# Kernel optimization log

Measured on AMD Instinct MI355X. Metric: run time of the kernel, lower is better.

## Reference

```python
import jax, jax.numpy as jnp
import numpy as np
import math

INF = 1e12  # constant.INFINITY_NUMBER in the original repo


def setup_inputs() -> dict:
    key = jax.random.key(0)
    ks = jax.random.split(key, 12)
    B, S, W, D = 16, 512, 8, 768
    M, Wm = 2, 64
    U, Wu = 32, 16
    V = 32000
    words = jax.random.randint(ks[0], (B, S, W), 0, V)
    masks = jax.random.randint(ks[1], (B, S, W), 0, 2).astype(bool)
    main = jax.random.randint(ks[2], (B, M, Wm), 0, V)
    main_mask = jax.random.randint(ks[3], (B, M, Wm), 0, 2).astype(bool)
    user = jax.random.randint(ks[4], (B, U, Wu), 0, V)
    user_mask = jax.random.randint(ks[5], (B, U, Wu), 0, 2).astype(bool)
    # sparse-ish dependency adjacency
    adj = (jax.random.uniform(ks[6], (B, S, S)) < 0.05).astype(jnp.float32)
    emb_weight = jax.random.normal(ks[7], (V, D), jnp.float32) * 0.02
    K_w = jax.random.normal(ks[8], (D, D), jnp.float32) * (1.0 / math.sqrt(D))
    K_b = jnp.zeros((D,), jnp.float32)
    Q_w = jax.random.normal(ks[9], (D, D), jnp.float32) * (1.0 / math.sqrt(D))
    Q_b = jnp.zeros((D,), jnp.float32)
    return {"words": words, "masks": masks, "main": main, "main_mask": main_mask,
            "user": user, "user_mask": user_mask, "adj": adj,
            "emb_weight": emb_weight, "K_w": K_w, "K_b": K_b, "Q_w": Q_w, "Q_b": Q_b}


def _masked_max(embs, mask, axis):
    # masked_fill(mask, -INF) -> max(axis) ; caller fixes residual -INF rows
    return jnp.max(jnp.where(mask[..., None], -INF, embs), axis=axis)


def reference(words, masks, main, main_mask, user, user_mask, adj,
              emb_weight, K_w, K_b, Q_w, Q_b):
    D = emb_weight.shape[1]

    word_embs = emb_weight[words]   # [B,S,W,D]
    main_embs = emb_weight[main]    # [B,M,Wm,D]
    user_embs = emb_weight[user]    # [B,U,Wu,D]

    # node mask from adjacency: True where node has no in/out edges
    mask = ((adj.sum(axis=2) + adj.sum(axis=1)) == 0)[:, :, None]  # [B,S,1]

    # main: masked max-pool over word pieces, zero fully-masked rows
    main_e = _masked_max(main_embs, main_mask, axis=2)             # [B,M,D]
    main_e = jnp.where(main_e == -INF, 0.0, main_e)

    # user: masked max-pool over word pieces then over users
    user_e = _masked_max(user_embs, user_mask, axis=2)             # [B,U,D]
    user_e = jnp.max(user_e, axis=1)                               # [B,D]
    user_e = jnp.where(user_e == -INF, 0.0, user_e)

    # token embeddings: masked max-pool over word pieces (no -INF fix in original)
    g = _masked_max(word_embs, masks, axis=2)                      # [B,S,D]

    # single-head attention: softmax(K g (Q g)^T / sqrt(D)) @ g
    key_ = g @ K_w.T + K_b                                         # [B,S,D]
    query = g @ Q_w.T + Q_b                                        # [B,S,D]
    scores = jnp.einsum('bsd,btd->bst', key_, query) / math.sqrt(D)
    dense_graph = jax.nn.softmax(scores, axis=2)                   # [B,S,S]
    gcn_out = jnp.einsum('bst,btd->bsd', dense_graph, g)           # [B,S,D]

    adj_sm = jax.nn.softmax(adj, axis=2)

    return (gcn_out, mask, dense_graph, adj_sm,
            jnp.squeeze(main_e), jnp.squeeze(user_e))
```

## Files before the change

kernel.cpp:

```cpp
#include <hip/hip_runtime.h>
#include <hip/hip_bf16.h>
#include <math.h>

static constexpr int Bn = 16, Sn = 512, Wn = 8, Dn = 768;
static constexpr int Mn_ = 2, WMn = 64;
static constexpr int Un = 32, WUn = 16;

#define INF_VAL 1e12f
#define INV_SQRT_D 0.03608439182435161f

static constexpr size_t OFF_GCN   = 0;
static constexpr size_t OFF_MASK  = 6291456;
static constexpr size_t OFF_DENSE = 6299648;
static constexpr size_t OFF_ADJ   = 10493952;
static constexpr size_t OFF_MAIN  = 14688256;
static constexpr size_t OFF_USER  = 14712832;

static constexpr size_t WSB_GBF     = 0;
static constexpr size_t WSB_GT      = 12582912;
static constexpr size_t WSB_DENSEBF = 25165824;
static constexpr size_t WSB_HBF     = 33554432;
static constexpr size_t WSB_KWT     = 46137344;
static constexpr size_t WSB_QWT     = 47316992;
static constexpr size_t WSB_MT      = 48496640;
static constexpr size_t WSB_PARTU   = 49676288;
static constexpr size_t WSB_PARTM   = 51249152;
static constexpr size_t WSB_KBAR    = 51642368;
static constexpr size_t WSB_QBAR    = 51648512;
static constexpr size_t WSB_U       = 51654656;
static constexpr size_t WSB_V       = 51660800;
static constexpr size_t WSB_VA      = 51666944;
static constexpr size_t WSB_VB      = 51673088;
static constexpr size_t WSB_CONSTS  = 51679232;
static constexpr size_t WSB_QS      = 51679296;
static constexpr size_t WSB_KQ      = 51712064;
static constexpr size_t WSB_GA      = 51744832;
static constexpr size_t WSB_GB      = 51777600;
static constexpr size_t WSB_COLSUM  = 51810368;
static constexpr size_t WSB_FLAGS   = 51843136;
static constexpr size_t WSB_ROWSUM  = 51875904;
static constexpr size_t WSB_UVU     = 51908672;
static constexpr size_t WSB_UVV     = 51957824;
static constexpr size_t WSB_UVA     = 52006976;
static constexpr size_t WSB_UVB     = 52056128;
static constexpr size_t WSB_RAWBF   = 52105280;

typedef __attribute__((ext_vector_type(8))) short short8;
typedef __attribute__((ext_vector_type(4))) float f32x4;

static __device__ __forceinline__ ushort f2bf(float f) {
    union { float f; unsigned u; } v; v.f = f;
    unsigned u = v.u;
    unsigned r = (u + 0x7FFFu + ((u >> 16) & 1u)) >> 16;
    return (ushort)r;
}

static __device__ __forceinline__ float bf2f(unsigned hi16) {
    union { unsigned u; float f; } v; v.u = hi16 << 16; return v.f;
}

static __device__ __forceinline__ void gload16(const void* g, void* lds) {
    __builtin_amdgcn_global_load_lds(
        (const __attribute__((address_space(1))) void*)g,
        (__attribute__((address_space(3))) void*)lds, 16, 0, 0);
}

static __device__ __forceinline__ void fmax4(float4& a, const float4& x) {
    a.x = fmaxf(a.x, x.x); a.y = fmaxf(a.y, x.y);
    a.z = fmaxf(a.z, x.z); a.w = fmaxf(a.w, x.w);
}

__global__ __launch_bounds__(256)
void fold1(const float* __restrict__ K_w, const float* __restrict__ K_b,
           const float* __restrict__ Q_w, const float* __restrict__ Q_b,
           double* __restrict__ kbar, double* __restrict__ qbar,
           ushort* __restrict__ KwbT, ushort* __restrict__ QwbT,
           float* __restrict__ colsum) {
    int blk = blockIdx.x, t = threadIdx.x;
    if (blk < 192) {
        int wv = t >> 6, lane = t & 63;
        int r = blk * 4 + wv;
        double sk = 0.0, sq = 0.0;
        for (int d = lane; d < Dn; d += 64) {
            sk += (double)K_w[(size_t)r * Dn + d];
            sq += (double)Q_w[(size_t)r * Dn + d];
        }
        #pragma unroll
        for (int off = 32; off > 0; off >>= 1) {
            sk += __shfl_down(sk, off, 64);
            sq += __shfl_down(sq, off, 64);
        }
        if (lane == 0) {
            kbar[r] = -1e12 * sk + (double)K_b[r];
            qbar[r] = -1e12 * sq + (double)Q_b[r];
        }
    } else if (blk < 1344) {
        int tt = blk - 192;
        const float* src = (tt < 576) ? K_w : Q_w;
        ushort* dst = (tt < 576) ? KwbT : QwbT;
        int t6 = (tt < 576) ? tt : tt - 576;
        int e0 = (t6 % 24) * 32, i0 = (t6 / 24) * 32;
        __shared__ ushort tile[32][33];
        int tx = t & 31, ty = t >> 5;
        #pragma unroll
        for (int i2 = 0; i2 < 4; ++i2)
            tile[ty + i2 * 8][tx] = f2bf(src[(size_t)(e0 + ty + i2 * 8) * Dn + i0 + tx]);
        __syncthreads();
        #pragma unroll
        for (int i2 = 0; i2 < 4; ++i2)
            dst[(size_t)(i0 + ty + i2 * 8) * Dn + e0 + tx] = tile[tx][ty + i2 * 8];
    } else {
        for (int i = t; i < Bn * Sn; i += 256) colsum[i] = 0.f;
    }
}

template<int OUT_BF16>
static __device__ __forceinline__
void gemm_device(const ushort* __restrict__ A, const ushort* __restrict__ B,
                 void* __restrict__ Cout, int bx, int by, int bz,
                 int Km, int lda, int ldb, int ldc,
                 long long sA, long long sB, long long sC,
                 ushort* As, ushort* Bs) {
    const ushort* Ab = A + (size_t)bz * sA;
    const ushort* Bb = B + (size_t)bz * sB;
    int i0 = by * 64, j0 = bx * 64;
    int tid = threadIdx.x;
    int lane = tid & 63, wv = tid >> 6;
    int wr = wv >> 1, wc = wv & 1;
    int ln15 = lane & 15, lkg = lane >> 4;
    int r4 = lane >> 4;
    int c16 = lane & 15;

    f32x4 acc[2][2] = {};

    for (int k0 = 0; k0 < Km; k0 += 128) {
        #pragma unroll
        for (int it = 0; it < 4; ++it) {
            int r = it * 16 + wv * 4 + r4;
            int cc = c16 ^ (r & 15);
            ushort* dstA = As + (it * 4096 + wv * 1024) / 2;
            gload16(Ab + (size_t)(i0 + r) * lda + k0 + cc * 8, dstA);
        }
        #pragma unroll
        for (int it = 0; it < 4; ++it) {
            int r = it * 16 + wv * 4 + r4;
            int cc = c16 ^ (r & 15);
            ushort* dstB = Bs + (it * 4096 + wv * 1024) / 2;
            gload16(Bb + (size_t)(j0 + r) * ldb + k0 + cc * 8, dstB);
        }
        __syncthreads();
        #pragma unroll
        for (int kh = 0; kh < 4; ++kh) {
            short8 af[2], bfr[2];
            int kc = kh * 4 + lkg;
            #pragma unroll
            for (int f = 0; f < 2; ++f) {
                int ra = wr * 32 + f * 16 + ln15;
                af[f] = *(const short8*)((const char*)As + ra * 256 + ((kc ^ (ra & 15)) << 4));
                int rb = wc * 32 + f * 16 + ln15;
                bfr[f] = *(const short8*)((const char*)Bs + rb * 256 + ((kc ^ (rb & 15)) << 4));
            }
            #pragma unroll
            for (int fa = 0; fa < 2; ++fa)
                #pragma unroll
                for (int fb = 0; fb < 2; ++fb)
                    acc[fa][fb] = __builtin_amdgcn_mfma_f32_16x16x32_bf16(
                        af[fa], bfr[fb], acc[fa][fb], 0, 0, 0);
        }
        __syncthreads();
    }

    #pragma unroll
    for (int fa = 0; fa < 2; ++fa) {
        #pragma unroll
        for (int fb = 0; fb < 2; ++fb) {
            int n = j0 + wc * 32 + fb * 16 + ln15;
            #pragma unroll
            for (int rr = 0; rr < 4; ++rr) {
                int m = i0 + wr * 32 + fa * 16 + lkg * 4 + rr;
                float val = acc[fa][fb][rr];
                if (OUT_BF16) {
                    ((ushort*)Cout)[(size_t)bz * sC + (size_t)m * ldc + n] = f2bf(val);
                } else {
                    ((float*)Cout)[(size_t)bz * sC + (size_t)m * ldc + n] = val;
                }
            }
        }
    }
}

template<int OUT_BF16>
__global__ __launch_bounds__(256)
void gemm_mfma(const ushort* __restrict__ A, const ushort* __restrict__ B,
               void* __restrict__ Cout,
               int Km, int lda, int ldb, int ldc,
               long long sA, long long sB, long long sC) {
    __shared__ ushort As[64 * 128];
    __shared__ ushort Bs[64 * 128];
    gemm_device<OUT_BF16>(A, B, Cout, blockIdx.x, blockIdx.y, blockIdx.z,
                          Km, lda, ldb, ldc, sA, sB, sC, As, Bs);
}

__global__ __launch_bounds__(256)
void adjuvmt_kernel(const float* __restrict__ adj, float* __restrict__ adjsm,
                    float* __restrict__ colsum, float* __restrict__ rowsum,
                    const float* __restrict__ K_w, const float* __restrict__ Q_w,
                    const float* __restrict__ K_b, const float* __restrict__ Q_b,
                    const double* __restrict__ kbar, const double* __restrict__ qbar,
                    double* __restrict__ uvu, double* __restrict__ uvv,
                    double* __restrict__ uva, double* __restrict__ uvb,
                    const ushort* __restrict__ QwbT, const ushort* __restrict__ KwbT,
                    ushort* __restrict__ Mt) {
    __shared__ ushort SB[16384];
    __shared__ float n1s[16];
    int blk = blockIdx.x;
    int t = threadIdx.x;
    if (blk < 24) {
        int id = blk * 256 + t;
        int c = id / 768;
        int j = id - c * 768;
        int e0 = c * 96;
        double su = 0.0, sv = 0.0, sa = 0.0, sb = 0.0;
        for (int e = e0; e < e0 + 96; ++e) {
            double kw = (double)K_w[(size_t)e * Dn + j];
            double qw = (double)Q_w[(size_t)e * Dn + j];
            su += kw * qbar[e];
            sv += qw * kbar[e];
            sa += kw * (double)Q_b[e];
            sb += qw * (double)K_b[e];
        }
        uvu[(size_t)c * Dn + j] = su;
        uvv[(size_t)c * Dn + j] = sv;
        uva[(size_t)c * Dn + j] = sa;
        uvb[(size_t)c * Dn + j] = sb;
        return;
    }
    if (blk < 168) {
        int g = blk - 24;
        gemm_device<1>(QwbT, KwbT, Mt, g % 12, g / 12, 0,
                       Dn, Dn, Dn, Dn, 0, 0, 0, SB, SB + 8192);
        return;
    }
    int ab = blk - 168;
    int b = ab >> 5, rc = ab & 31;
    const float* base = adj + ((size_t)b * Sn + rc * 16) * Sn;
    float* obase = adjsm + ((size_t)b * Sn + rc * 16) * Sn;
    const float EM1 = 0.36787944117144233f;
    const float EP1 = 2.718281828459045f;
    float (*rows)[512] = (float(*)[512])SB;
    #pragma unroll
    for (int r = 0; r < 16; ++r) {
        rows[r][t]       = base[(size_t)r * Sn + t];
        rows[r][t + 256] = base[(size_t)r * Sn + t + 256];
    }
    __syncthreads();
    int wv = t >> 6, lane = t & 63;
    #pragma unroll
    for (int rr2 = 0; rr2 < 4; ++rr2) {
        int r = wv * 4 + rr2;
        float s = 0.f;
        #pragma unroll
        for (int c = 0; c < 8; ++c) s += rows[r][lane + c * 64];
        #pragma unroll
        for (int off = 32; off > 0; off >>= 1) s += __shfl_down(s, off, 64);
        if (lane == 0) {
            n1s[r] = s;
            rowsum[(size_t)b * Sn + rc * 16 + r] = s;
        }
    }
    __syncthreads();
    float colacc0 = 0.f, colacc1 = 0.f;
    #pragma unroll
    for (int r = 0; r < 16; ++r) {
        float a0 = rows[r][t], a1 = rows[r][t + 256];
        colacc0 += a0; colacc1 += a1;
        float n1 = n1s[r];
        float e1, e0;
        if (n1 > 0.f) { e1 = 1.f; e0 = EM1; } else { e1 = EP1; e0 = 1.f; }
        float inv = 1.f / (n1 * e1 + (512.f - n1) * e0);
        obase[(size_t)r * Sn + t]       = (a0 == 1.f ? e1 : e0) * inv;
        obase[(size_t)r * Sn + t + 256] = (a1 == 1.f ? e1 : e0) * inv;
    }
    atomicAdd(&colsum[(size_t)b * Sn + t], colacc0);
    atomicAdd(&colsum[(size_t)b * Sn + t + 256], colacc1);
}

__global__ __launch_bounds__(64)
void uvred_consts(const double* __restrict__ uvu, const double* __restrict__ uvv,
                  const double* __restrict__ uva, const double* __restrict__ uvb,
                  const double* __restrict__ kbar, const double* __restrict__ qbar,
                  const float* __restrict__ K_b, const float* __restrict__ Q_b,
                  double* __restrict__ u, double* __restrict__ v,
                  double* __restrict__ va, double* __restrict__ vb,
                  double* __restrict__ consts) {
    int blk = blockIdx.x;
    int l = threadIdx.x;
    if (blk < 12) {
        int j = blk * 64 + l;
        double su = 0.0, sv = 0.0, sa = 0.0, sb = 0.0;
        #pragma unroll
        for (int c = 0; c < 8; ++c) {
            su += uvu[(size_t)c * Dn + j];
            sv += uvv[(size_t)c * Dn + j];
            sa += uva[(size_t)c * Dn + j];
            sb += uvb[(size_t)c * Dn + j];
        }
        u[j] = su; v[j] = sv; va[j] = sa; vb[j] = sb;
    } else {
        double c0 = 0.0, c1 = 0.0, c2 = 0.0, c3 = 0.0;
        for (int e = l; e < Dn; e += 64) {
            c0 += kbar[e] * (double)Q_b[e];
            c1 += kbar[e] * qbar[e];
            c2 += qbar[e] * (double)K_b[e];
            c3 += (double)K_b[e] * (double)Q_b[e];
        }
        #pragma unroll
        for (int off = 32; off > 0; off >>= 1) {
            c0 += __shfl_down(c0, off, 64);
            c1 += __shfl_down(c1, off, 64);
            c2 += __shfl_down(c2, off, 64);
            c3 += __shfl_down(c3, off, 64);
        }
        if (l == 0) { consts[0] = c0; consts[1] = c1; consts[2] = c2; consts[3] = c3; }
    }
}

__global__ __launch_bounds__(192)
void pool_g_s1(const int* __restrict__ words, const int* __restrict__ masks,
               const int* __restrict__ main_idx, const int* __restrict__ mmask,
               const int* __restrict__ user_idx, const int* __restrict__ umask,
               const float* __restrict__ emb,
               const double* __restrict__ u, const double* __restrict__ v,
               const double* __restrict__ va, const double* __restrict__ vb,
               const double* __restrict__ consts,
               ushort* __restrict__ gbf, float* __restrict__ qs,
               float* __restrict__ kq, float* __restrict__ ga,
               float* __restrict__ gb, int* __restrict__ flags,
               float* __restrict__ partM, float* __restrict__ partU) {
    int blk = blockIdx.x;
    int t = threadIdx.x;
    if (blk >= Bn * Sn) {
        int s1 = blk - Bn * Sn;
        const int *irow, *mrow;
        float* dst;
        if (s1 < 128) {
            int bm = s1 >> 2, ch = s1 & 3;
            irow = main_idx + (size_t)bm * WMn + ch * 16;
            mrow = mmask + (size_t)bm * WMn + ch * 16;
            dst = partM + (size_t)s1 * Dn;
        } else {
            int bu = s1 - 128;
            irow = user_idx + (size_t)bu * WUn;
            mrow = umask + (size_t)bu * WUn;
            dst = partU + (size_t)bu * Dn;
        }
        float4 acc = make_float4(-INF_VAL, -INF_VAL, -INF_VAL, -INF_VAL);
        #pragma unroll
        for (int w = 0; w < 16; ++w) {
            if (mrow[w] != 0) continue;
            float4 x = ((const float4*)(emb + (size_t)irow[w] * Dn))[t];
            fmax4(acc, x);
        }
        ((float4*)dst)[t] = acc;
        return;
    }
    int bs = blk;
    const int* wrow = words + (size_t)bs * Wn;
    const int* mrow = masks + (size_t)bs * Wn;
    float4 acc = make_float4(-INF_VAL, -INF_VAL, -INF_VAL, -INF_VAL);
    int nm = 0;
    #pragma unroll
    for (int w = 0; w < Wn; ++w) {
        int mk = mrow[w];
        nm += (mk != 0);
        if (mk != 0) continue;
        float4 x = ((const float4*)(emb + (size_t)wrow[w] * Dn))[t];
        fmax4(acc, x);
    }
    ushort4 o;
    o.x = f2bf(acc.x); o.y = f2bf(acc.y); o.z = f2bf(acc.z); o.w = f2bf(acc.w);
    ((ushort4*)(gbf + (size_t)bs * Dn))[t] = o;
    int j = t * 4;
    double dv = v[j] * (double)acc.x + v[j+1] * (double)acc.y
              + v[j+2] * (double)acc.z + v[j+3] * (double)acc.w;
    double du = u[j] * (double)acc.x + u[j+1] * (double)acc.y
              + u[j+2] * (double)acc.z + u[j+3] * (double)acc.w;
    double da = va[j] * (double)acc.x + va[j+1] * (double)acc.y
              + va[j+2] * (double)acc.z + va[j+3] * (double)acc.w;
    double db = vb[j] * (double)acc.x + vb[j+1] * (double)acc.y
              + vb[j+2] * (double)acc.z + vb[j+3] * (double)acc.w;
    #pragma unroll
    for (int off = 32; off > 0; off >>= 1) {
        dv += __shfl_down(dv, off, 64);
        du += __shfl_down(du, off, 64);
        da += __shfl_down(da, off, 64);
        db += __shfl_down(db, off, 64);
    }
    __shared__ double rr[12];
    if ((t & 63) == 0) {
        rr[t >> 6] = dv; rr[3 + (t >> 6)] = du;
        rr[6 + (t >> 6)] = da; rr[9 + (t >> 6)] = db;
    }
    __syncthreads();
    if (t == 0) {
        qs[bs] = (float)(rr[0] + rr[1] + rr[2] + consts[0]);
        kq[bs] = (float)(rr[3] + rr[4] + rr[5] + consts[2]);
        ga[bs] = (float)(rr[6] + rr[7] + rr[8]);
        gb[bs] = (float)(rr[9] + rr[10] + rr[11]);
        flags[bs] = (nm == Wn) ? 1 : 0;
    }
}

__global__ __launch_bounds__(256)
void midh_kernel(const ushort* __restrict__ gbf, const ushort* __restrict__ Mt,
                 ushort* __restrict__ hbf, ushort* __restrict__ gT,
                 const float* __restrict__ partM, const float* __restrict__ partU,
                 float* __restrict__ outM, float* __restrict__ outU,
                 const float* __restrict__ rowsum, const float* __restrict__ colsum,
                 float* __restrict__ maskout) {
    __shared__ ushort SB[16384];
    int blk = blockIdx.x;
    int t = threadIdx.x;
    if (blk < 1536) {
        gemm_device<1>(gbf, Mt, hbf, blk % 12, blk / 12, 0,
                       Dn, Dn, Dn, Dn, 0, 0, 0, SB, SB + 8192);
        return;
    }
    if (blk < 7680) {
        int bb = blk - 1536;
        ushort (*tile)[33] = (ushort(*)[33])SB;
        int b = bb / 384;
        int rem = bb - b * 384;
        int d0 = (rem % 24) * 32, s0 = (rem / 24) * 32;
        int tx = t & 31, ty = t >> 5;
        #pragma unroll
        for (int i = 0; i < 4; ++i)
            tile[ty + i * 8][tx] = gbf[((size_t)(b * Sn + s0 + ty + i * 8)) * Dn + d0 + tx];
        __syncthreads();
        #pragma unroll
        for (int i = 0; i < 4; ++i)
            gT[((size_t)(b * Dn + d0 + ty + i * 8)) * Sn + s0 + tx] = tile[tx][ty + i * 8];
        return;
    }
    if (blk >= 7728) {
        int i = (blk - 7728) * 256 + t;
        if (i < Bn * Sn)
            maskout[i] = ((rowsum[i] + colsum[i]) == 0.f) ? 1.f : 0.f;
        return;
    }
    if (t >= 192) return;
    float4 acc = make_float4(-INF_VAL, -INF_VAL, -INF_VAL, -INF_VAL);
    float* dst;
    if (blk < 7712) {
        int bm = blk - 7680;
        #pragma unroll
        for (int c = 0; c < 4; ++c) {
            float4 x = ((const float4*)(partM + (size_t)(bm * 4 + c) * Dn))[t];
            fmax4(acc, x);
        }
        dst = outM + (size_t)bm * Dn;
    } else {
        int b = blk - 7712;
        for (int u2 = 0; u2 < Un; ++u2) {
            float4 x = ((const float4*)(partU + (size_t)(b * Un + u2) * Dn))[t];
            fmax4(acc, x);
        }
        dst = outU + (size_t)b * Dn;
    }
    if (acc.x == -INF_VAL) acc.x = 0.f;
    if (acc.y == -INF_VAL) acc.y = 0.f;
    if (acc.z == -INF_VAL) acc.z = 0.f;
    if (acc.w == -INF_VAL) acc.w = 0.f;
    ((float4*)dst)[t] = acc;
}

__global__ __launch_bounds__(256)
void softmax_fix(const ushort* __restrict__ raw, const int* __restrict__ flags,
                 const float* __restrict__ qs, const float* __restrict__ kq,
                 const float* __restrict__ ga, const float* __restrict__ gb,
                 const double* __restrict__ consts,
                 float* __restrict__ dense, ushort* __restrict__ densebf) {
    int bs = blockIdx.x;
    int b = bs >> 9;
    int t = threadIdx.x;
    int c0i = 2 * t, c1idx = 2 * t + 1;
    unsigned rpack = ((const unsigned*)(raw + (size_t)bs * 512))[t];
    float r0 = bf2f(rpack & 0xFFFFu);
    float r1 = bf2f(rpack >> 16);
    int f0 = flags[(b << 9) + c0i];
    int f1 = flags[(b << 9) + c1idx];
    bool sm = flags[bs] != 0;
    float x0, x1;
    if (sm) {
        float c1v = (float)consts[1] * INV_SQRT_D;
        x0 = f0 ? c1v : qs[(b << 9) + c0i] * INV_SQRT_D;
        x1 = f1 ? c1v : qs[(b << 9) + c1idx] * INV_SQRT_D;
    } else {
        float kqi = kq[bs] * INV_SQRT_D;
        float corr = ga[bs] + (float)consts[3];
        x0 = f0 ? kqi : (r0 + corr + gb[(b << 9) + c0i]) * INV_SQRT_D;
        x1 = f1 ? kqi : (r1 + corr + gb[(b << 9) + c1idx]) * INV_SQRT_D;
    }
    float m = fmaxf(x0, x1);
    #pragma unroll
    for (int off = 32; off > 0; off >>= 1) m = fmaxf(m, __shfl_down(m, off, 64));
    __shared__ float red[4];
    __shared__ float bmax, bsum;
    if ((t & 63) == 0) red[t >> 6] = m;
    __syncthreads();
    if (t == 0) bmax = fmaxf(fmaxf(red[0], red[1]), fmaxf(red[2], red[3]));
    __syncthreads();
    float mx = bmax;
    float e0 = expf(x0 - mx), e1 = expf(x1 - mx);
    float s = e0 + e1;
    #pragma unroll
    for (int off = 32; off > 0; off >>= 1) s += __shfl_down(s, off, 64);
    if ((t & 63) == 0) red[t >> 6] = s;
    __syncthreads();
    if (t == 0) bsum = red[0] + red[1] + red[2] + red[3];
    __syncthreads();
    float inv = 1.f / bsum;
    float p0 = e0 * inv, p1 = e1 * inv;
    float2 pv; pv.x = p0; pv.y = p1;
    ((float2*)(dense + (size_t)bs * 512))[t] = pv;
    ((unsigned*)(densebf + (size_t)bs * 512))[t] =
        (unsigned)f2bf(p0) | ((unsigned)f2bf(p1) << 16);
}

extern "C" void kernel_launch(void* const* d_in, const int* in_sizes, int n_in,
                              void* d_out, int out_size, void* d_ws, size_t ws_size,
                              hipStream_t stream) {
    const int*   words     = (const int*)d_in[0];
    const int*   masks     = (const int*)d_in[1];
    const int*   main_idx  = (const int*)d_in[2];
    const int*   main_mask = (const int*)d_in[3];
    const int*   user_idx  = (const int*)d_in[4];
    const int*   user_mask = (const int*)d_in[5];
    const float* adj       = (const float*)d_in[6];
    const float* emb       = (const float*)d_in[7];
    const float* K_w       = (const float*)d_in[8];
    const float* K_b       = (const float*)d_in[9];
    const float* Q_w       = (const float*)d_in[10];
    const float* Q_b       = (const float*)d_in[11];

    float* out = (float*)d_out;
    char*  ws8 = (char*)d_ws;

    ushort* gbf     = (ushort*)(ws8 + WSB_GBF);
    ushort* gT      = (ushort*)(ws8 + WSB_GT);
    ushort* densebf = (ushort*)(ws8 + WSB_DENSEBF);
    ushort* hbf     = (ushort*)(ws8 + WSB_HBF);
    ushort* KwbT    = (ushort*)(ws8 + WSB_KWT);
    ushort* QwbT    = (ushort*)(ws8 + WSB_QWT);
    ushort* Mt      = (ushort*)(ws8 + WSB_MT);
    ushort* rawbf   = (ushort*)(ws8 + WSB_RAWBF);
    float*  partU   = (float*)(ws8 + WSB_PARTU);
    float*  partM   = (float*)(ws8 + WSB_PARTM);
    double* kbar    = (double*)(ws8 + WSB_KBAR);
    double* qbar    = (double*)(ws8 + WSB_QBAR);
    double* u       = (double*)(ws8 + WSB_U);
    double* v       = (double*)(ws8 + WSB_V);
    double* va      = (double*)(ws8 + WSB_VA);
    double* vb      = (double*)(ws8 + WSB_VB);
    double* consts  = (double*)(ws8 + WSB_CONSTS);
    float*  qs      = (float*)(ws8 + WSB_QS);
    float*  kq      = (float*)(ws8 + WSB_KQ);
    float*  ga      = (float*)(ws8 + WSB_GA);
    float*  gb      = (float*)(ws8 + WSB_GB);
    float*  colsum  = (float*)(ws8 + WSB_COLSUM);
    int*    flags   = (int*)(ws8 + WSB_FLAGS);
    float*  rowsum  = (float*)(ws8 + WSB_ROWSUM);
    double* uvu     = (double*)(ws8 + WSB_UVU);
    double* uvv     = (double*)(ws8 + WSB_UVV);
    double* uva     = (double*)(ws8 + WSB_UVA);
    double* uvb     = (double*)(ws8 + WSB_UVB);

    float* dense = out + OFF_DENSE;

    fold1<<<1345, 256, 0, stream>>>(K_w, K_b, Q_w, Q_b, kbar, qbar, KwbT, QwbT, colsum);

    adjuvmt_kernel<<<680, 256, 0, stream>>>(adj, out + OFF_ADJ, colsum, rowsum,
                                            K_w, Q_w, K_b, Q_b, kbar, qbar,
                                            uvu, uvv, uva, uvb, QwbT, KwbT, Mt);

    uvred_consts<<<13, 64, 0, stream>>>(uvu, uvv, uva, uvb, kbar, qbar, K_b, Q_b,
                                        u, v, va, vb, consts);

    pool_g_s1<<<Bn * Sn + 640, 192, 0, stream>>>(
        words, masks, main_idx, main_mask, user_idx, user_mask, emb,
        u, v, va, vb, consts, gbf, qs, kq, ga, gb, flags, partM, partU);

    midh_kernel<<<7760, 256, 0, stream>>>(gbf, Mt, hbf, gT, partM, partU,
                                          out + OFF_MAIN, out + OFF_USER,
                                          rowsum, colsum, out + OFF_MASK);

    gemm_mfma<1><<<dim3(8, 8, Bn), 256, 0, stream>>>(
        hbf, gbf, rawbf, Dn, Dn, Dn, Sn,
        (long long)Sn * Dn, (long long)Sn * Dn, (long long)Sn * Sn);

    softmax_fix<<<Bn * Sn, 256, 0, stream>>>(rawbf, flags, qs, kq, ga, gb, consts,
                                             dense, densebf);

    gemm_mfma<0><<<dim3(12, 8, Bn), 256, 0, stream>>>(
        densebf, gT, out + OFF_GCN, Sn, Sn, Sn, Dn,
        (long long)Sn * Sn, (long long)Dn * Sn, (long long)Sn * Dn);
}
```

Baseline: 142.3 us.

## Fuse score GEMM with softmax into a single full-row kernel

Replaces the separate score GEMM (which wrote bf16 raw scores to workspace) and the row softmax kernel with one kernel. Each block computes a 16x512 strip of scores with MFMA, applies the flag-based fixups, and does the row softmax in registers and LDS. This removes the raw-score round trip and one launch. In exchange only 512 blocks run, B operands are read straight from global with no LDS staging or reuse, and dense outputs are written as scalar stores, which can cost bandwidth and occupancy.

```diff
diff --git a/kernel.cpp b/kernel.cpp
--- a/kernel.cpp
+++ b/kernel.cpp
@@ -43,7 +43,6 @@
 static constexpr size_t WSB_UVV     = 51957824;
 static constexpr size_t WSB_UVA     = 52006976;
 static constexpr size_t WSB_UVB     = 52056128;
-static constexpr size_t WSB_RAWBF   = 52105280;
 
 typedef __attribute__((ext_vector_type(8))) short short8;
 typedef __attribute__((ext_vector_type(4))) float f32x4;
@@ -53,10 +52,6 @@
     unsigned u = v.u;
     unsigned r = (u + 0x7FFFu + ((u >> 16) & 1u)) >> 16;
     return (ushort)r;
-}
-
-static __device__ __forceinline__ float bf2f(unsigned hi16) {
-    union { unsigned u; float f; } v; v.u = hi16 << 16; return v.f;
 }
 
 static __device__ __forceinline__ void gload16(const void* g, void* lds) {
@@ -475,56 +470,126 @@
 }
 
 __global__ __launch_bounds__(256)
-void softmax_fix(const ushort* __restrict__ raw, const int* __restrict__ flags,
-                 const float* __restrict__ qs, const float* __restrict__ kq,
-                 const float* __restrict__ ga, const float* __restrict__ gb,
-                 const double* __restrict__ consts,
-                 float* __restrict__ dense, ushort* __restrict__ densebf) {
-    int bs = blockIdx.x;
-    int b = bs >> 9;
+void scoresm_kernel(const ushort* __restrict__ hbf, const ushort* __restrict__ gbf,
+                    const int* __restrict__ flags, const float* __restrict__ qs,
+                    const float* __restrict__ kq, const float* __restrict__ ga,
+                    const float* __restrict__ gb, const double* __restrict__ consts,
+                    float* __restrict__ dense, ushort* __restrict__ densebf) {
+    __shared__ ushort As[16 * 768];
+    __shared__ float smax[4][16];
+    __shared__ float ssum[4][16];
+    int b = blockIdx.y;
+    int r0 = blockIdx.x * 16;
     int t = threadIdx.x;
-    int c0i = 2 * t, c1idx = 2 * t + 1;
-    unsigned rpack = ((const unsigned*)(raw + (size_t)bs * 512))[t];
-    float r0 = bf2f(rpack & 0xFFFFu);
-    float r1 = bf2f(rpack >> 16);
-    int f0 = flags[(b << 9) + c0i];
-    int f1 = flags[(b << 9) + c1idx];
-    bool sm = flags[bs] != 0;
-    float x0, x1;
-    if (sm) {
-        float c1v = (float)consts[1] * INV_SQRT_D;
-        x0 = f0 ? c1v : qs[(b << 9) + c0i] * INV_SQRT_D;
-        x1 = f1 ? c1v : qs[(b << 9) + c1idx] * INV_SQRT_D;
-    } else {
-        float kqi = kq[bs] * INV_SQRT_D;
-        float corr = ga[bs] + (float)consts[3];
-        x0 = f0 ? kqi : (r0 + corr + gb[(b << 9) + c0i]) * INV_SQRT_D;
-        x1 = f1 ? kqi : (r1 + corr + gb[(b << 9) + c1idx]) * INV_SQRT_D;
-    }
-    float m = fmaxf(x0, x1);
-    #pragma unroll
-    for (int off = 32; off > 0; off >>= 1) m = fmaxf(m, __shfl_down(m, off, 64));
-    __shared__ float red[4];
-    __shared__ float bmax, bsum;
-    if ((t & 63) == 0) red[t >> 6] = m;
+    int lane = t & 63, wv = t >> 6;
+    int ln15 = lane & 15, lkg = lane >> 4;
+
+    const ushort* Ab = hbf + ((size_t)b * Sn + r0) * Dn;
+    for (int i = t; i < 1536; i += 256) {
+        int r = i / 96, c = i - (i / 96) * 96;
+        int cs = (c & ~15) | ((c & 15) ^ r);
+        *(short8*)((char*)As + (r * 96 + cs) * 16) =
+            *(const short8*)((const char*)Ab + (size_t)r * Dn * 2 + c * 16);
+    }
     __syncthreads();
-    if (t == 0) bmax = fmaxf(fmaxf(red[0], red[1]), fmaxf(red[2], red[3]));
+
+    const ushort* Bb = gbf + (size_t)b * Sn * Dn;
+    f32x4 acc[8] = {};
+    for (int s = 0; s < 24; ++s) {
+        int kc = s * 4 + lkg;
+        int cs = (kc & ~15) | ((kc & 15) ^ ln15);
+        short8 af = *(const short8*)((char*)As + (ln15 * 96 + cs) * 16);
+        #pragma unroll
+        for (int nf = 0; nf < 8; ++nf) {
+            int n = wv * 128 + nf * 16 + ln15;
+            short8 bf = *(const short8*)((const char*)Bb + ((size_t)n * Dn + kc * 8) * 2);
+            acc[nf] = __builtin_amdgcn_mfma_f32_16x16x32_bf16(af, bf, acc[nf], 0, 0, 0);
+        }
+    }
+
+    float c1v = (float)consts[1] * INV_SQRT_D;
+    float c3v = (float)consts[3];
+    int rowflag[4]; float kqv[4], gav[4];
+    #pragma unroll
+    for (int rr2 = 0; rr2 < 4; ++rr2) {
+        int row = (b << 9) + r0 + lkg * 4 + rr2;
+        rowflag[rr2] = flags[row];
+        kqv[rr2] = kq[row] * INV_SQRT_D;
+        gav[rr2] = ga[row] + c3v;
+    }
+    #pragma unroll
+    for (int nf = 0; nf < 8; ++nf) {
+        int col = wv * 128 + nf * 16 + ln15;
+        int fcol = flags[(b << 9) + col];
+        float qscol = qs[(b << 9) + col] * INV_SQRT_D;
+        float gbcol = gb[(b << 9) + col];
+        #pragma unroll
+        for (int rr2 = 0; rr2 < 4; ++rr2) {
+            float x;
+            if (rowflag[rr2]) {
+                x = fcol ? c1v : qscol;
+            } else {
+                x = fcol ? kqv[rr2]
+                         : (acc[nf][rr2] + gav[rr2] + gbcol) * INV_SQRT_D;
+            }
+            acc[nf][rr2] = x;
+        }
+    }
+
+    float mx[4];
+    #pragma unroll
+    for (int rr2 = 0; rr2 < 4; ++rr2) {
+        float m = acc[0][rr2];
+        #pragma unroll
+        for (int nf = 1; nf < 8; ++nf) m = fmaxf(m, acc[nf][rr2]);
+        #pragma unroll
+        for (int msk = 1; msk < 16; msk <<= 1) m = fmaxf(m, __shfl_xor(m, msk, 64));
+        mx[rr2] = m;
+        if (ln15 == 0) smax[wv][lkg * 4 + rr2] = m;
+    }
     __syncthreads();
-    float mx = bmax;
-    float e0 = expf(x0 - mx), e1 = expf(x1 - mx);
-    float s = e0 + e1;
-    #pragma unroll
-    for (int off = 32; off > 0; off >>= 1) s += __shfl_down(s, off, 64);
-    if ((t & 63) == 0) red[t >> 6] = s;
+    #pragma unroll
+    for (int rr2 = 0; rr2 < 4; ++rr2) {
+        int m_ = lkg * 4 + rr2;
+        mx[rr2] = fmaxf(fmaxf(smax[0][m_], smax[1][m_]),
+                        fmaxf(smax[2][m_], smax[3][m_]));
+    }
+
+    float sm[4] = {0.f, 0.f, 0.f, 0.f};
+    #pragma unroll
+    for (int nf = 0; nf < 8; ++nf)
+        #pragma unroll
+        for (int rr2 = 0; rr2 < 4; ++rr2) {
+            float e = expf(acc[nf][rr2] - mx[rr2]);
+            acc[nf][rr2] = e;
+            sm[rr2] += e;
+        }
+    #pragma unroll
+    for (int rr2 = 0; rr2 < 4; ++rr2) {
+        float s2 = sm[rr2];
+        #pragma unroll
+        for (int msk = 1; msk < 16; msk <<= 1) s2 += __shfl_xor(s2, msk, 64);
+        if (ln15 == 0) ssum[wv][lkg * 4 + rr2] = s2;
+    }
     __syncthreads();
-    if (t == 0) bsum = red[0] + red[1] + red[2] + red[3];
-    __syncthreads();
-    float inv = 1.f / bsum;
-    float p0 = e0 * inv, p1 = e1 * inv;
-    float2 pv; pv.x = p0; pv.y = p1;
-    ((float2*)(dense + (size_t)bs * 512))[t] = pv;
-    ((unsigned*)(densebf + (size_t)bs * 512))[t] =
-        (unsigned)f2bf(p0) | ((unsigned)f2bf(p1) << 16);
+    float inv[4];
+    #pragma unroll
+    for (int rr2 = 0; rr2 < 4; ++rr2) {
+        int m_ = lkg * 4 + rr2;
+        inv[rr2] = 1.f / (ssum[0][m_] + ssum[1][m_] + ssum[2][m_] + ssum[3][m_]);
+    }
+
+    #pragma unroll
+    for (int nf = 0; nf < 8; ++nf) {
+        int col = wv * 128 + nf * 16 + ln15;
+        #pragma unroll
+        for (int rr2 = 0; rr2 < 4; ++rr2) {
+            size_t rowg = (size_t)(b << 9) + r0 + lkg * 4 + rr2;
+            float p = acc[nf][rr2] * inv[rr2];
+            dense[rowg * 512 + col] = p;
+            densebf[rowg * 512 + col] = f2bf(p);
+        }
+    }
 }
 
 extern "C" void kernel_launch(void* const* d_in, const int* in_sizes, int n_in,
@@ -553,7 +618,6 @@
     ushort* KwbT    = (ushort*)(ws8 + WSB_KWT);
     ushort* QwbT    = (ushort*)(ws8 + WSB_QWT);
     ushort* Mt      = (ushort*)(ws8 + WSB_MT);
-    ushort* rawbf   = (ushort*)(ws8 + WSB_RAWBF);
     float*  partU   = (float*)(ws8 + WSB_PARTU);
     float*  partM   = (float*)(ws8 + WSB_PARTM);
     double* kbar    = (double*)(ws8 + WSB_KBAR);
@@ -594,12 +658,8 @@
                                           out + OFF_MAIN, out + OFF_USER,
                                           rowsum, colsum, out + OFF_MASK);
 
-    gemm_mfma<1><<<dim3(8, 8, Bn), 256, 0, stream>>>(
-        hbf, gbf, rawbf, Dn, Dn, Dn, Sn,
-        (long long)Sn * Dn, (long long)Sn * Dn, (long long)Sn * Sn);
-
-    softmax_fix<<<Bn * Sn, 256, 0, stream>>>(rawbf, flags, qs, kq, ga, gb, consts,
-                                             dense, densebf);
+    scoresm_kernel<<<dim3(32, Bn), 256, 0, stream>>>(
+        hbf, gbf, flags, qs, kq, ga, gb, consts, dense, densebf);
 
     gemm_mfma<0><<<dim3(12, 8, Bn), 256, 0, stream>>>(
         densebf, gT, out + OFF_GCN, Sn, Sn, Sn, Dn,
```

Measured after the change: 161.0 us. +13.1%, slower.
